# Kernel optimization log

Measured on AMD Instinct MI355X. Metric: run time of the kernel, lower is better.

Reference implementation:

```python
import jax, jax.numpy as jnp
import numpy as np

B, D, H = 16384, 32, 512


def _init_linear(key, fan_in, fan_out):
    k1, k2 = jax.random.split(key)
    lim = 1.0 / np.sqrt(fan_in)
    W = jax.random.uniform(k1, (fan_in, fan_out), jnp.float32, -lim, lim)
    b = jax.random.uniform(k2, (fan_out,), jnp.float32, -lim, lim)
    return W, b


def setup_inputs() -> dict:
    key = jax.random.key(0)
    ks = jax.random.split(key, 8)
    q = jax.random.normal(ks[0], (B, D), jnp.float32)
    p = jax.random.normal(ks[1], (B, D), jnp.float32)
    t = jax.random.uniform(ks[2], (B, 1), jnp.float32)
    dt = jnp.float32(0.1)
    W0, b0 = _init_linear(ks[3], D + 1, H)
    W1, b1 = _init_linear(ks[4], H + 1, H)
    W2, b2 = _init_linear(ks[5], H + 1, H)
    W3, b3 = _init_linear(ks[6], H + 1, H)
    Wout, bout = _init_linear(ks[7], H + 1, D * D)
    return {"q": q, "p": p, "t": t, "dt": dt,
            "W0": W0, "b0": b0, "W1": W1, "b1": b1, "W2": W2, "b2": b2,
            "W3": W3, "b3": b3, "Wout": Wout, "bout": bout}


def _time_injection_net(x, t, Ws, bs):
    # concat time each layer, selu on all but last (matches TimeInjectionNet.forward)
    n = len(Ws)
    for i, (W, b) in enumerate(zip(Ws, bs)):
        x = jnp.concatenate((x, t), axis=1)
        x = x @ W + b
        if i < n - 1:
            x = jax.nn.selu(x)
    return x


def reference(q, p, t, dt, W0, b0, W1, b1, W2, b2, W3, b3, Wout, bout):
    # Q-term integrate_step: matrix from p, integrate q
    Ws = (W0, W1, W2, W3, Wout)
    bs = (b0, b1, b2, b3, bout)
    flat = _time_injection_net(p, t, Ws, bs)           # [B, D*D]
    dense = jnp.clip(flat.reshape(-1, D, D), -20.0, 20.0)  # [B, D, D]
    expm = jax.vmap(jax.scipy.linalg.expm)(dt * dense)  # batched matrix exponential
    new_q = jnp.einsum('bij,bj->bi', expm, q)           # [B, D]
    dlogp = dt * jnp.trace(dense, axis1=1, axis2=2)     # [B]
    return new_q, dlogp
```

## Files before the change

kernel.cpp:

```cpp
#include <hip/hip_runtime.h>
#include <hip/hip_bf16.h>
#include <math.h>

#define BTOT 16384

typedef __attribute__((ext_vector_type(8))) short short8;
typedef __attribute__((ext_vector_type(4))) float f32x4;
typedef __attribute__((ext_vector_type(16))) float f32x16;

__device__ __forceinline__ float selu_fast(float x) {
  const float scale = 1.0507009873554805f;
  const float alpha = 1.6732632423543772f;
  float e = exp2f(x * 1.44269504088896f);
  float neg = alpha * (e - 1.0f);
  return scale * (x > 0.0f ? x : neg);
}

__device__ __forceinline__ unsigned int bf16u(float x) {
  __hip_bfloat16 h = __float2bfloat16(x);
  return (unsigned int)*reinterpret_cast<unsigned short*>(&h);
}

__global__ __launch_bounds__(256) void prep_kernel(
    const float* __restrict__ W0, unsigned int* __restrict__ Wf0,
    const float* __restrict__ W1, unsigned int* __restrict__ Wf1,
    const float* __restrict__ W2, unsigned int* __restrict__ Wf2,
    const float* __restrict__ W3, unsigned int* __restrict__ Wf3,
    const float* __restrict__ Wout, unsigned int* __restrict__ WfO) {
  __shared__ float tile[32][33];
  const int t = blockIdx.x;
  const float* W;
  unsigned int* Wf;
  int N, TS, kbt, nbt;
  if (t < 16)        { W = W0;   Wf = Wf0; N = 512;  TS = 1;  kbt = 0;       nbt = t; }
  else if (t < 272)  { int u = t - 16;  W = W1;   Wf = Wf1; N = 512;  TS = 16; kbt = u & 15; nbt = u >> 4; }
  else if (t < 528)  { int u = t - 272; W = W2;   Wf = Wf2; N = 512;  TS = 16; kbt = u & 15; nbt = u >> 4; }
  else if (t < 784)  { int u = t - 528; W = W3;   Wf = Wf3; N = 512;  TS = 16; kbt = u & 15; nbt = u >> 4; }
  else               { int u = t - 784; W = Wout; Wf = WfO; N = 1024; TS = 16; kbt = u & 15; nbt = u >> 4; }
  const int kb32 = kbt * 32, nb32 = nbt * 32;
  const int tx = threadIdx.x & 31, ty = threadIdx.x >> 5;
  #pragma unroll
  for (int rr = 0; rr < 4; ++rr) {
    int kl = ty + rr * 8;
    tile[kl][tx] = W[(size_t)(kb32 + kl) * N + nb32 + tx];
  }
  __syncthreads();
  const int cbb = threadIdx.x >> 7;
  const int rest = threadIdx.x & 127;
  const int l = rest >> 1;
  const int wjh = rest & 1;
  const int cb = 2 * nbt + cbb;
  unsigned int wv[2];
  #pragma unroll
  for (int m = 0; m < 2; ++m) {
    int wj = wjh * 2 + m;
    int kl = (l >> 4) * 8 + wj * 2;
    int nl = cbb * 16 + (l & 15);
    wv[m] = bf16u(tile[kl][nl]) | (bf16u(tile[kl + 1][nl]) << 16);
  }
  size_t widx = ((size_t)(cb * TS + kbt) * 64 + l) * 4 + wjh * 2;
  *reinterpret_cast<uint2*>(Wf + widx) = make_uint2(wv[0], wv[1]);
}

template<int K, int N, int MODE>
__device__ __forceinline__ void run_layer(
    const short8* __restrict__ Wf,
    const float* __restrict__ Wlast,
    const float* __restrict__ bias,
    char* actBuf,
    __hip_bfloat16* __restrict__ gOut, int rowbase,
    const float* tsl, int w, int lane) {
  constexpr int TS = K / 32;
  constexpr int NKB = K / 8;
  constexpr int PASSES = N / 512;
  const int colloc = lane & 15, kg = lane >> 4;
  int rbyte[2], rmask[2];
  #pragma unroll
  for (int i = 0; i < 2; ++i) {
    int r = i * 16 + colloc;
    rbyte[i] = r * 1024;
    rmask[i] = r & (NKB - 1);
  }
  #pragma unroll 1
  for (int pass = 0; pass < PASSES; ++pass) {
    const int wb = pass * 512 + w * 32;
    const int cb0 = wb >> 4;
    f32x4 acc[2][2] = {};
    short8 acur[2], bcur0, bcur1;
    bcur0 = Wf[(size_t)(cb0 * TS) * 64 + lane];
    bcur1 = Wf[(size_t)((cb0 + 1) * TS) * 64 + lane];
    #pragma unroll
    for (int i = 0; i < 2; ++i)
      acur[i] = *reinterpret_cast<const short8*>(actBuf + rbyte[i] + ((kg ^ rmask[i]) * 16));
    #pragma unroll 2
    for (int t = 0; t < TS; ++t) {
      const int tn = (t + 1 < TS) ? (t + 1) : t;
      short8 bnx0 = Wf[(size_t)(cb0 * TS + tn) * 64 + lane];
      short8 bnx1 = Wf[(size_t)((cb0 + 1) * TS + tn) * 64 + lane];
      short8 anx[2];
      #pragma unroll
      for (int i = 0; i < 2; ++i)
        anx[i] = *reinterpret_cast<const short8*>(actBuf + rbyte[i] + (((tn * 4 + kg) ^ rmask[i]) * 16));
      #pragma unroll
      for (int i = 0; i < 2; ++i) {
        acc[i][0] = __builtin_amdgcn_mfma_f32_16x16x32_bf16(acur[i], bcur0, acc[i][0], 0, 0, 0);
        acc[i][1] = __builtin_amdgcn_mfma_f32_16x16x32_bf16(acur[i], bcur1, acc[i][1], 0, 0, 0);
      }
      #pragma unroll
      for (int i = 0; i < 2; ++i) acur[i] = anx[i];
      bcur0 = bnx0; bcur1 = bnx1;
    }
    if (MODE == 0) __syncthreads();
    float wl[2], bb[2];
    #pragma unroll
    for (int c = 0; c < 2; ++c) {
      int col = wb + c * 16 + colloc;
      wl[c] = Wlast[col];
      bb[c] = bias[col];
    }
    #pragma unroll
    for (int i = 0; i < 2; ++i) {
      #pragma unroll
      for (int e = 0; e < 4; ++e) {
        int row = i * 16 + kg * 4 + e;
        float tv = tsl[row];
        #pragma unroll
        for (int c = 0; c < 2; ++c) {
          float v = acc[i][c][e] + tv * wl[c] + bb[c];
          if (MODE == 0) {
            v = selu_fast(v);
            int col = wb + c * 16 + colloc;
            int off = row * 1024 + (((col >> 3) ^ (row & 63)) * 16) + (col & 7) * 2;
            *reinterpret_cast<unsigned short*>(actBuf + off) =
                (unsigned short)bf16u(v);
          } else {
            v = fminf(fmaxf(v, -20.f), 20.f);
            float o = __shfl_xor(v, 1);
            unsigned int me = bf16u(v), ot = bf16u(o);
            unsigned int pw = (colloc & 1) ? ((me << 16) | ot) : ((ot << 16) | me);
            const bool iwrite = ((colloc & 1) == (e >> 1));
            int col0 = wb + c * 16 + (colloc & ~1);
            if (iwrite) {
              size_t off = (size_t)(rowbase + row) * N + col0;
              *reinterpret_cast<unsigned int*>(
                  reinterpret_cast<char*>(gOut) + off * 2) = pw;
            }
          }
        }
      }
    }
  }
}

__global__ __launch_bounds__(1024) void fused_mlp_kernel(
    const float* __restrict__ p,
    const float* __restrict__ tvec,
    const short8* Wf0, const short8* Wf1, const short8* Wf2,
    const short8* Wf3, const short8* WfO,
    const float* W0l, const float* b0,
    const float* W1l, const float* b1,
    const float* W2l, const float* b2,
    const float* W3l, const float* b3,
    const float* WOl, const float* bO,
    __hip_bfloat16* __restrict__ flatb) {
  __shared__ char buf[32768];
  __shared__ float tsl[32];
  const int tid = threadIdx.x;
  const int w = tid >> 6, lane = tid & 63;
  const int rowbase = blockIdx.x * 32;

  if (tid < 32) tsl[tid] = tvec[rowbase + tid];
  if (tid < 256) {
    const int r = tid >> 3, g = tid & 7;
    float4 v = *reinterpret_cast<const float4*>(p + (size_t)(rowbase + r) * 32 + g * 4);
    unsigned int lo = bf16u(v.x) | (bf16u(v.y) << 16);
    unsigned int hi = bf16u(v.z) | (bf16u(v.w) << 16);
    int off = r * 1024 + (((g >> 1) ^ (r & 3)) * 16) + (g & 1) * 8;
    *reinterpret_cast<uint2*>(buf + off) = make_uint2(lo, hi);
  }
  __syncthreads();

  run_layer<32, 512, 0>(Wf0, W0l, b0, buf, nullptr, rowbase, tsl, w, lane);
  __syncthreads();
  run_layer<512, 512, 0>(Wf1, W1l, b1, buf, nullptr, rowbase, tsl, w, lane);
  __syncthreads();
  run_layer<512, 512, 0>(Wf2, W2l, b2, buf, nullptr, rowbase, tsl, w, lane);
  __syncthreads();
  run_layer<512, 512, 0>(Wf3, W3l, b3, buf, nullptr, rowbase, tsl, w, lane);
  __syncthreads();
  run_layer<512, 1024, 1>(WfO, WOl, bO, buf, flatb, rowbase, tsl, w, lane);
}

#define WAITLDS asm volatile("s_waitcnt lgkmcnt(0)" ::: "memory")

__device__ __forceinline__ unsigned int bf16r(float x) {
  return (__float_as_uint(x) + 0x8000u) >> 16;
}

__device__ __forceinline__ void d2b_lean(const float (&X)[16], int G, short8 (&bfr)[2]) {
  float rcv[8];
  #pragma unroll
  for (int j = 0; j < 8; ++j) {
    const int hp = j >> 2, tt = j & 3;
    float snd = G ? X[8 * hp + tt] : X[8 * hp + 4 + tt];
    rcv[j] = __shfl_xor(snd, 32);
  }
  #pragma unroll
  for (int h = 0; h < 2; ++h) {
    float r8v[8];
    #pragma unroll
    for (int j2 = 0; j2 < 8; ++j2) {
      if (j2 < 4) r8v[j2] = G ? rcv[4 * h + j2] : X[8 * h + j2];
      else        r8v[j2] = G ? X[8 * h + j2] : rcv[4 * h + j2 - 4];
    }
    union { short8 s8; unsigned int u[4]; } bu;
    #pragma unroll
    for (int j = 0; j < 4; ++j)
      bu.u[j] = bf16r(r8v[2 * j]) | (bf16r(r8v[2 * j + 1]) << 16);
    bfr[h] = bu.s8;
  }
}

__device__ __forceinline__ void d2b_split_lean(const float (&X)[16], int G,
                                               short8 (&bh)[2], short8 (&bl)[2]) {
  float rcv[8];
  #pragma unroll
  for (int j = 0; j < 8; ++j) {
    const int hp = j >> 2, tt = j & 3;
    float snd = G ? X[8 * hp + tt] : X[8 * hp + 4 + tt];
    rcv[j] = __shfl_xor(snd, 32);
  }
  #pragma unroll
  for (int h = 0; h < 2; ++h) {
    float r8v[8];
    #pragma unroll
    for (int j2 = 0; j2 < 8; ++j2) {
      if (j2 < 4) r8v[j2] = G ? rcv[4 * h + j2] : X[8 * h + j2];
      else        r8v[j2] = G ? X[8 * h + j2] : rcv[4 * h + j2 - 4];
    }
    union { short8 s8; unsigned int u[4]; } uh, ul;
    #pragma unroll
    for (int j = 0; j < 4; ++j) {
      unsigned int b0 = __float_as_uint(r8v[2 * j]) & 0xFFFF0000u;
      unsigned int b1 = __float_as_uint(r8v[2 * j + 1]) & 0xFFFF0000u;
      float l0 = r8v[2 * j] - __uint_as_float(b0);
      float l1 = r8v[2 * j + 1] - __uint_as_float(b1);
      uh.u[j] = (b0 >> 16) | b1;
      ul.u[j] = bf16r(l0) | (bf16r(l1) << 16);
    }
    bh[h] = uh.s8;
    bl[h] = ul.s8;
  }
}

union u4s8 { uint4 u4; short8 s8; unsigned int u[4]; };

__global__ __launch_bounds__(256) void expm_ilp2_kernel(
    const __hip_bfloat16* __restrict__ flat,
    const float* __restrict__ q,
    const float* __restrict__ dtp,
    float* __restrict__ out_q,
    float* __restrict__ out_dlogp) {
  __shared__ __align__(16) unsigned int SL[4][2][16][33];
  const int tid = threadIdx.x;
  const int w = tid >> 6, lane = tid & 63;
  const int C = lane & 31, G = lane >> 5;
  const int m0 = blockIdx.x * 8 + w * 2;
  const float dt = dtp[0];

  u4s8 t0[2], t1[2];
  float E[2][16];
  float uu[2];
  int nv[2];

  #pragma unroll
  for (int mm = 0; mm < 2; ++mm) {
    const int m = m0 + mm;
    const uint4* fm = reinterpret_cast<const uint4*>(flat + (size_t)m * 1024);
    uint4 v0 = fm[lane];
    uint4 v1 = fm[lane + 64];
    {
      const int r0 = lane >> 2, kpb = (lane & 3) * 4;
      SL[w][mm][kpb + 0][r0] = v0.x; SL[w][mm][kpb + 1][r0] = v0.y;
      SL[w][mm][kpb + 2][r0] = v0.z; SL[w][mm][kpb + 3][r0] = v0.w;
      SL[w][mm][kpb + 0][r0 + 16] = v1.x; SL[w][mm][kpb + 1][r0 + 16] = v1.y;
      SL[w][mm][kpb + 2][r0 + 16] = v1.z; SL[w][mm][kpb + 3][r0 + 16] = v1.w;
    }
    {
      const char* base = reinterpret_cast<const char*>(flat) + (size_t)m * 2048 + C * 64 + G * 16;
      t0[mm].u4 = *reinterpret_cast<const uint4*>(base);
      t1[mm].u4 = *reinterpret_cast<const uint4*>(base + 32);
    }

    float sa = 0.f;
    #pragma unroll
    for (int i = 0; i < 4; ++i) {
      sa += fabsf(__uint_as_float(t0[mm].u[i] << 16)) + fabsf(__uint_as_float(t0[mm].u[i] & 0xFFFF0000u));
      sa += fabsf(__uint_as_float(t1[mm].u[i] << 16)) + fabsf(__uint_as_float(t1[mm].u[i] & 0xFFFF0000u));
    }
    sa += __shfl_xor(sa, 32);
    float nrm = sa;
    #pragma unroll
    for (int off = 1; off < 32; off <<= 1) nrm = fmaxf(nrm, __shfl_xor(nrm, off));

    int s = 0;
    float anrm = dt * nrm;
    if (anrm > 1.0f) {
      s = (int)ceilf(log2f(anrm));
      s = s < 1 ? 1 : (s > 6 ? 6 : s);
    }
    nv[mm] = 1 << s;
    const float u = dt * exp2f(-(float)s);
    uu[mm] = u;

    unsigned int pt0[4], pt1[4];
    #pragma unroll
    for (int d = 0; d < 4; ++d) {
      pt0[d] = (unsigned int)__shfl_xor((int)t0[mm].u[d], 32);
      pt1[d] = (unsigned int)__shfl_xor((int)t1[mm].u[d], 32);
    }
    float tr = 0.f;
    #pragma unroll
    for (int j = 0; j < 4; ++j) {
      #pragma unroll
      for (int e2 = 0; e2 < 4; ++e2) {
        const int i = 4 * j + e2;
        const int rd = e2 + 8 * j + 4 * G;
        const bool own = ((j & 1) == G);
        unsigned int dwO, dwP;
        if ((e2 >> 1) == 0) {
          dwO = G ? ((j < 2) ? t0[mm].u[2] : t1[mm].u[2]) : ((j < 2) ? t0[mm].u[0] : t1[mm].u[0]);
          dwP = G ? ((j < 2) ? pt0[2] : pt1[2]) : ((j < 2) ? pt0[0] : pt1[0]);
        } else {
          dwO = G ? ((j < 2) ? t0[mm].u[3] : t1[mm].u[3]) : ((j < 2) ? t0[mm].u[1] : t1[mm].u[1]);
          dwP = G ? ((j < 2) ? pt0[3] : pt1[3]) : ((j < 2) ? pt0[1] : pt1[1]);
        }
        unsigned int dw = own ? dwO : dwP;
        unsigned int h16 = (e2 & 1) ? (dw >> 16) : (dw & 0xFFFFu);
        float mv = __uint_as_float(h16 << 16);
        float dI = (rd == C) ? 1.0f : 0.0f;
        E[mm][i] = dI + u * mv;
        tr += dI * mv;
      }
    }
    #pragma unroll
    for (int off = 1; off < 64; off <<= 1) tr += __shfl_xor(tr, off);
    if (lane == 0) out_dlogp[m] = dt * tr;
  }

  WAITLDS;

  short8 Mfr[2][2];
  {
    const unsigned int selpat = (C & 1) ? 0x07060302u : 0x05040100u;
    #pragma unroll
    for (int mm = 0; mm < 2; ++mm) {
      #pragma unroll
      for (int h = 0; h < 2; ++h) {
        unsigned int rr[8];
        #pragma unroll
        for (int e = 0; e < 8; ++e) rr[e] = SL[w][mm][C >> 1][16 * h + 8 * G + e];
        union { short8 s8; unsigned int u[4]; } mu;
        #pragma unroll
        for (int j = 0; j < 4; ++j)
          mu.u[j] = __builtin_amdgcn_perm(rr[2 * j + 1], rr[2 * j], selpat);
        Mfr[mm][h] = mu.s8;
      }
    }
  }

  float Qc[2][16];
  float ck[2];
  #pragma unroll
  for (int mm = 0; mm < 2; ++mm) {
    ck[mm] = uu[mm] * uu[mm] * 0.5f;
    f32x16 acc = {};
    acc = __builtin_amdgcn_mfma_f32_32x32x16_bf16(Mfr[mm][0], t0[mm].s8, acc, 0, 0, 0);
    acc = __builtin_amdgcn_mfma_f32_32x32x16_bf16(Mfr[mm][1], t1[mm].s8, acc, 0, 0, 0);
    #pragma unroll
    for (int i = 0; i < 16; ++i) { Qc[mm][i] = acc[i]; E[mm][i] += ck[mm] * acc[i]; }
  }
  #pragma unroll
  for (int k = 3; k <= 6; ++k) {
    #pragma unroll
    for (int mm = 0; mm < 2; ++mm) {
      short8 bfr[2];
      d2b_lean(Qc[mm], G, bfr);
      f32x16 acc = {};
      acc = __builtin_amdgcn_mfma_f32_32x32x16_bf16(Mfr[mm][0], bfr[0], acc, 0, 0, 0);
      acc = __builtin_amdgcn_mfma_f32_32x32x16_bf16(Mfr[mm][1], bfr[1], acc, 0, 0, 0);
      ck[mm] *= uu[mm] * (1.0f / (float)k);
      #pragma unroll
      for (int i = 0; i < 16; ++i) { Qc[mm][i] = acc[i]; E[mm][i] += ck[mm] * acc[i]; }
    }
  }

  short8 beh[2][2], bel[2][2];
  #pragma unroll
  for (int mm = 0; mm < 2; ++mm)
    d2b_split_lean(E[mm], G, beh[mm], bel[mm]);

  float qv[2];
  qv[0] = q[(size_t)m0 * 32 + C];
  qv[1] = q[(size_t)(m0 + 1) * 32 + C];
  const int nvmax = nv[0] > nv[1] ? nv[0] : nv[1];
  #pragma unroll 1
  for (int it = 0; it < nvmax; ++it) {
    #pragma unroll
    for (int mm = 0; mm < 2; ++mm) {
      unsigned int hb = __float_as_uint(qv[mm]) & 0xFFFF0000u;
      float lof = qv[mm] - __uint_as_float(hb);
      unsigned int pw = (hb >> 16) | (bf16r(lof) << 16);
      short8 vh[2], vl[2];
      #pragma unroll
      for (int h = 0; h < 2; ++h) {
        unsigned int g[8];
        #pragma unroll
        for (int e = 0; e < 8; ++e)
          g[e] = (unsigned int)__shfl((int)pw, 16 * h + 8 * G + e);
        union { short8 s8; unsigned int u[4]; } uh, ul;
        #pragma unroll
        for (int j = 0; j < 4; ++j) {
          uh.u[j] = __builtin_amdgcn_perm(g[2 * j + 1], g[2 * j], 0x05040100u);
          ul.u[j] = __builtin_amdgcn_perm(g[2 * j + 1], g[2 * j], 0x07060302u);
        }
        vh[h] = uh.s8;
        vl[h] = ul.s8;
      }
      f32x16 acc = {};
      acc = __builtin_amdgcn_mfma_f32_32x32x16_bf16(vh[0], beh[mm][0], acc, 0, 0, 0);
      acc = __builtin_amdgcn_mfma_f32_32x32x16_bf16(vh[1], beh[mm][1], acc, 0, 0, 0);
      acc = __builtin_amdgcn_mfma_f32_32x32x16_bf16(vl[0], beh[mm][0], acc, 0, 0, 0);
      acc = __builtin_amdgcn_mfma_f32_32x32x16_bf16(vl[1], beh[mm][1], acc, 0, 0, 0);
      acc = __builtin_amdgcn_mfma_f32_32x32x16_bf16(vh[0], bel[mm][0], acc, 0, 0, 0);
      acc = __builtin_amdgcn_mfma_f32_32x32x16_bf16(vh[1], bel[mm][1], acc, 0, 0, 0);
      qv[mm] = (it < nv[mm]) ? acc[0] : qv[mm];
    }
  }
  if (G == 0) {
    out_q[(size_t)m0 * 32 + C] = qv[0];
    out_q[(size_t)(m0 + 1) * 32 + C] = qv[1];
  }
}

extern "C" void kernel_launch(void* const* d_in, const int* in_sizes, int n_in,
                              void* d_out, int out_size, void* d_ws, size_t ws_size,
                              hipStream_t stream) {
  const float* q    = (const float*)d_in[0];
  const float* p    = (const float*)d_in[1];
  const float* t    = (const float*)d_in[2];
  const float* dt   = (const float*)d_in[3];
  const float* W0   = (const float*)d_in[4];
  const float* b0   = (const float*)d_in[5];
  const float* W1   = (const float*)d_in[6];
  const float* b1   = (const float*)d_in[7];
  const float* W2   = (const float*)d_in[8];
  const float* b2   = (const float*)d_in[9];
  const float* W3   = (const float*)d_in[10];
  const float* b3   = (const float*)d_in[11];
  const float* Wout = (const float*)d_in[12];
  const float* bout = (const float*)d_in[13];

  char* ws = (char*)d_ws;
  __hip_bfloat16* flatb = (__hip_bfloat16*)ws;
  unsigned int* Wf0 = (unsigned int*)(ws + (size_t)BTOT * 1024 * 2);
  unsigned int* Wf1 = Wf0 + 32 * 512 / 2;
  unsigned int* Wf2 = Wf1 + 512 * 512 / 2;
  unsigned int* Wf3 = Wf2 + 512 * 512 / 2;
  unsigned int* WfO = Wf3 + 512 * 512 / 2;

  prep_kernel<<<1296, 256, 0, stream>>>(W0, Wf0, W1, Wf1, W2, Wf2, W3, Wf3,
                                        Wout, WfO);

  fused_mlp_kernel<<<512, 1024, 0, stream>>>(
      p, t,
      (const short8*)Wf0, (const short8*)Wf1, (const short8*)Wf2,
      (const short8*)Wf3, (const short8*)WfO,
      W0 + 32 * 512, b0, W1 + 512 * 512, b1, W2 + 512 * 512, b2,
      W3 + 512 * 512, b3, Wout + 512 * 1024, bout, flatb);

  float* out_q     = (float*)d_out;
  float* out_dlogp = out_q + (size_t)BTOT * 32;
  expm_ilp2_kernel<<<BTOT / 8, 256, 0, stream>>>(flatb, q, dt, out_q, out_dlogp);
}
```

Measured before the change: 119.5 us.

## Fuse MLP and batched matrix exponential into one kernel via LDS handoff

```diff
diff --git a/kernel.cpp b/kernel.cpp
--- a/kernel.cpp
+++ b/kernel.cpp
@@ -20,6 +20,12 @@
   __hip_bfloat16 h = __float2bfloat16(x);
   return (unsigned int)*reinterpret_cast<unsigned short*>(&h);
 }
+
+__device__ __forceinline__ unsigned int bf16r(float x) {
+  return (__float_as_uint(x) + 0x8000u) >> 16;
+}
+
+union u4s8 { uint4 u4; short8 s8; unsigned int u[4]; };
 
 __global__ __launch_bounds__(256) void prep_kernel(
     const float* __restrict__ W0, unsigned int* __restrict__ Wf0,
@@ -67,8 +73,7 @@
     const short8* __restrict__ Wf,
     const float* __restrict__ Wlast,
     const float* __restrict__ bias,
-    char* actBuf,
-    __hip_bfloat16* __restrict__ gOut, int rowbase,
+    char* actBuf, char* flatL,
     const float* tsl, int w, int lane) {
   constexpr int TS = K / 32;
   constexpr int NKB = K / 8;
@@ -140,11 +145,8 @@
             unsigned int pw = (colloc & 1) ? ((me << 16) | ot) : ((ot << 16) | me);
             const bool iwrite = ((colloc & 1) == (e >> 1));
             int col0 = wb + c * 16 + (colloc & ~1);
-            if (iwrite) {
-              size_t off = (size_t)(rowbase + row) * N + col0;
-              *reinterpret_cast<unsigned int*>(
-                  reinterpret_cast<char*>(gOut) + off * 2) = pw;
-            }
+            if (iwrite)
+              *reinterpret_cast<unsigned int*>(flatL + (size_t)row * 2048 + col0 * 2) = pw;
           }
         }
       }
@@ -152,7 +154,65 @@
   }
 }
 
-__global__ __launch_bounds__(1024) void fused_mlp_kernel(
+__device__ __forceinline__ void d2b_lean(const float (&X)[16], int G, short8 (&bfr)[2]) {
+  float rcv[8];
+  #pragma unroll
+  for (int j = 0; j < 8; ++j) {
+    const int hp = j >> 2, tt = j & 3;
+    float snd = G ? X[8 * hp + tt] : X[8 * hp + 4 + tt];
+    rcv[j] = __shfl_xor(snd, 32);
+  }
+  #pragma unroll
+  for (int h = 0; h < 2; ++h) {
+    float r8v[8];
+    #pragma unroll
+    for (int j2 = 0; j2 < 8; ++j2) {
+      if (j2 < 4) r8v[j2] = G ? rcv[4 * h + j2] : X[8 * h + j2];
+      else        r8v[j2] = G ? X[8 * h + j2] : rcv[4 * h + j2 - 4];
+    }
+    union { short8 s8; unsigned int u[4]; } bu;
+    #pragma unroll
+    for (int j = 0; j < 4; ++j)
+      bu.u[j] = bf16r(r8v[2 * j]) | (bf16r(r8v[2 * j + 1]) << 16);
+    bfr[h] = bu.s8;
+  }
+}
+
+__device__ __forceinline__ void d2b_split_lean(const float (&X)[16], int G,
+                                               short8 (&bh)[2], short8 (&bl)[2]) {
+  float rcv[8];
+  #pragma unroll
+  for (int j = 0; j < 8; ++j) {
+    const int hp = j >> 2, tt = j & 3;
+    float snd = G ? X[8 * hp + tt] : X[8 * hp + 4 + tt];
+    rcv[j] = __shfl_xor(snd, 32);
+  }
+  #pragma unroll
+  for (int h = 0; h < 2; ++h) {
+    float r8v[8];
+    #pragma unroll
+    for (int j2 = 0; j2 < 8; ++j2) {
+      if (j2 < 4) r8v[j2] = G ? rcv[4 * h + j2] : X[8 * h + j2];
+      else        r8v[j2] = G ? X[8 * h + j2] : rcv[4 * h + j2 - 4];
+    }
+    union { short8 s8; unsigned int u[4]; } uh, ul;
+    #pragma unroll
+    for (int j = 0; j < 4; ++j) {
+      unsigned int b0 = __float_as_uint(r8v[2 * j]) & 0xFFFF0000u;
+      unsigned int b1 = __float_as_uint(r8v[2 * j + 1]) & 0xFFFF0000u;
+      float l0 = r8v[2 * j] - __uint_as_float(b0);
+      float l1 = r8v[2 * j + 1] - __uint_as_float(b1);
+      uh.u[j] = (b0 >> 16) | b1;
+      ul.u[j] = bf16r(l0) | (bf16r(l1) << 16);
+    }
+    bh[h] = uh.s8;
+    bl[h] = ul.s8;
+  }
+}
+
+#define WAITLDS asm volatile("s_waitcnt lgkmcnt(0)" ::: "memory")
+
+__global__ __launch_bounds__(1024) void mega_kernel(
     const float* __restrict__ p,
     const float* __restrict__ tvec,
     const short8* Wf0, const short8* Wf1, const short8* Wf2,
@@ -162,9 +222,15 @@
     const float* W2l, const float* b2,
     const float* W3l, const float* b3,
     const float* WOl, const float* bO,
-    __hip_bfloat16* __restrict__ flatb) {
-  __shared__ char buf[32768];
+    const float* __restrict__ q,
+    const float* __restrict__ dtp,
+    float* __restrict__ out_q,
+    float* __restrict__ out_dlogp) {
+  __shared__ char actflat[98304];
+  __shared__ __align__(16) unsigned int slab[16 * 16 * 33];
   __shared__ float tsl[32];
+  char* act = actflat;
+  char* flatL = actflat + 32768;
   const int tid = threadIdx.x;
   const int w = tid >> 6, lane = tid & 63;
   const int rowbase = blockIdx.x * 32;
@@ -176,118 +242,47 @@
     unsigned int lo = bf16u(v.x) | (bf16u(v.y) << 16);
     unsigned int hi = bf16u(v.z) | (bf16u(v.w) << 16);
     int off = r * 1024 + (((g >> 1) ^ (r & 3)) * 16) + (g & 1) * 8;
-    *reinterpret_cast<uint2*>(buf + off) = make_uint2(lo, hi);
-  }
-  __syncthreads();
-
-  run_layer<32, 512, 0>(Wf0, W0l, b0, buf, nullptr, rowbase, tsl, w, lane);
-  __syncthreads();
-  run_layer<512, 512, 0>(Wf1, W1l, b1, buf, nullptr, rowbase, tsl, w, lane);
-  __syncthreads();
-  run_layer<512, 512, 0>(Wf2, W2l, b2, buf, nullptr, rowbase, tsl, w, lane);
-  __syncthreads();
-  run_layer<512, 512, 0>(Wf3, W3l, b3, buf, nullptr, rowbase, tsl, w, lane);
-  __syncthreads();
-  run_layer<512, 1024, 1>(WfO, WOl, bO, buf, flatb, rowbase, tsl, w, lane);
-}
-
-#define WAITLDS asm volatile("s_waitcnt lgkmcnt(0)" ::: "memory")
-
-__device__ __forceinline__ unsigned int bf16r(float x) {
-  return (__float_as_uint(x) + 0x8000u) >> 16;
-}
-
-__device__ __forceinline__ void d2b_lean(const float (&X)[16], int G, short8 (&bfr)[2]) {
-  float rcv[8];
-  #pragma unroll
-  for (int j = 0; j < 8; ++j) {
-    const int hp = j >> 2, tt = j & 3;
-    float snd = G ? X[8 * hp + tt] : X[8 * hp + 4 + tt];
-    rcv[j] = __shfl_xor(snd, 32);
-  }
-  #pragma unroll
-  for (int h = 0; h < 2; ++h) {
-    float r8v[8];
-    #pragma unroll
-    for (int j2 = 0; j2 < 8; ++j2) {
-      if (j2 < 4) r8v[j2] = G ? rcv[4 * h + j2] : X[8 * h + j2];
-      else        r8v[j2] = G ? X[8 * h + j2] : rcv[4 * h + j2 - 4];
-    }
-    union { short8 s8; unsigned int u[4]; } bu;
-    #pragma unroll
-    for (int j = 0; j < 4; ++j)
-      bu.u[j] = bf16r(r8v[2 * j]) | (bf16r(r8v[2 * j + 1]) << 16);
-    bfr[h] = bu.s8;
-  }
-}
-
-__device__ __forceinline__ void d2b_split_lean(const float (&X)[16], int G,
-                                               short8 (&bh)[2], short8 (&bl)[2]) {
-  float rcv[8];
-  #pragma unroll
-  for (int j = 0; j < 8; ++j) {
-    const int hp = j >> 2, tt = j & 3;
-    float snd = G ? X[8 * hp + tt] : X[8 * hp + 4 + tt];
-    rcv[j] = __shfl_xor(snd, 32);
-  }
-  #pragma unroll
-  for (int h = 0; h < 2; ++h) {
-    float r8v[8];
-    #pragma unroll
-    for (int j2 = 0; j2 < 8; ++j2) {
-      if (j2 < 4) r8v[j2] = G ? rcv[4 * h + j2] : X[8 * h + j2];
-      else        r8v[j2] = G ? X[8 * h + j2] : rcv[4 * h + j2 - 4];
-    }
-    union { short8 s8; unsigned int u[4]; } uh, ul;
-    #pragma unroll
-    for (int j = 0; j < 4; ++j) {
-      unsigned int b0 = __float_as_uint(r8v[2 * j]) & 0xFFFF0000u;
-      unsigned int b1 = __float_as_uint(r8v[2 * j + 1]) & 0xFFFF0000u;
-      float l0 = r8v[2 * j] - __uint_as_float(b0);
-      float l1 = r8v[2 * j + 1] - __uint_as_float(b1);
-      uh.u[j] = (b0 >> 16) | b1;
-      ul.u[j] = bf16r(l0) | (bf16r(l1) << 16);
-    }
-    bh[h] = uh.s8;
-    bl[h] = ul.s8;
-  }
-}
-
-union u4s8 { uint4 u4; short8 s8; unsigned int u[4]; };
-
-__global__ __launch_bounds__(256) void expm_ilp2_kernel(
-    const __hip_bfloat16* __restrict__ flat,
-    const float* __restrict__ q,
-    const float* __restrict__ dtp,
-    float* __restrict__ out_q,
-    float* __restrict__ out_dlogp) {
-  __shared__ __align__(16) unsigned int SL[4][2][16][33];
-  const int tid = threadIdx.x;
-  const int w = tid >> 6, lane = tid & 63;
+    *reinterpret_cast<uint2*>(act + off) = make_uint2(lo, hi);
+  }
+  __syncthreads();
+
+  run_layer<32, 512, 0>(Wf0, W0l, b0, act, nullptr, tsl, w, lane);
+  __syncthreads();
+  run_layer<512, 512, 0>(Wf1, W1l, b1, act, nullptr, tsl, w, lane);
+  __syncthreads();
+  run_layer<512, 512, 0>(Wf2, W2l, b2, act, nullptr, tsl, w, lane);
+  __syncthreads();
+  run_layer<512, 512, 0>(Wf3, W3l, b3, act, nullptr, tsl, w, lane);
+  __syncthreads();
+  run_layer<512, 1024, 1>(WfO, WOl, bO, act, flatL, tsl, w, lane);
+  __syncthreads();
+
   const int C = lane & 31, G = lane >> 5;
-  const int m0 = blockIdx.x * 8 + w * 2;
   const float dt = dtp[0];
+  unsigned int* SW = slab + w * (16 * 33);
 
   u4s8 t0[2], t1[2];
   float E[2][16];
   float uu[2];
   int nv[2];
+  short8 Mfr[2][2];
 
   #pragma unroll
   for (int mm = 0; mm < 2; ++mm) {
-    const int m = m0 + mm;
-    const uint4* fm = reinterpret_cast<const uint4*>(flat + (size_t)m * 1024);
-    uint4 v0 = fm[lane];
-    uint4 v1 = fm[lane + 64];
+    const int mloc = w * 2 + mm;
+    const int m = rowbase + mloc;
+    const uint4* fmL = reinterpret_cast<const uint4*>(flatL + (size_t)mloc * 2048);
+    uint4 v0 = fmL[lane];
+    uint4 v1 = fmL[lane + 64];
     {
       const int r0 = lane >> 2, kpb = (lane & 3) * 4;
-      SL[w][mm][kpb + 0][r0] = v0.x; SL[w][mm][kpb + 1][r0] = v0.y;
-      SL[w][mm][kpb + 2][r0] = v0.z; SL[w][mm][kpb + 3][r0] = v0.w;
-      SL[w][mm][kpb + 0][r0 + 16] = v1.x; SL[w][mm][kpb + 1][r0 + 16] = v1.y;
-      SL[w][mm][kpb + 2][r0 + 16] = v1.z; SL[w][mm][kpb + 3][r0 + 16] = v1.w;
+      SW[(kpb + 0) * 33 + r0] = v0.x; SW[(kpb + 1) * 33 + r0] = v0.y;
+      SW[(kpb + 2) * 33 + r0] = v0.z; SW[(kpb + 3) * 33 + r0] = v0.w;
+      SW[(kpb + 0) * 33 + r0 + 16] = v1.x; SW[(kpb + 1) * 33 + r0 + 16] = v1.y;
+      SW[(kpb + 2) * 33 + r0 + 16] = v1.z; SW[(kpb + 3) * 33 + r0 + 16] = v1.w;
     }
     {
-      const char* base = reinterpret_cast<const char*>(flat) + (size_t)m * 2048 + C * 64 + G * 16;
+      const char* base = flatL + (size_t)mloc * 2048 + C * 64 + G * 16;
       t0[mm].u4 = *reinterpret_cast<const uint4*>(base);
       t1[mm].u4 = *reinterpret_cast<const uint4*>(base + 32);
     }
@@ -346,20 +341,15 @@
     #pragma unroll
     for (int off = 1; off < 64; off <<= 1) tr += __shfl_xor(tr, off);
     if (lane == 0) out_dlogp[m] = dt * tr;
-  }
-
-  WAITLDS;
-
-  short8 Mfr[2][2];
-  {
-    const unsigned int selpat = (C & 1) ? 0x07060302u : 0x05040100u;
-    #pragma unroll
-    for (int mm = 0; mm < 2; ++mm) {
+
+    WAITLDS;
+    {
+      const unsigned int selpat = (C & 1) ? 0x07060302u : 0x05040100u;
       #pragma unroll
       for (int h = 0; h < 2; ++h) {
         unsigned int rr[8];
         #pragma unroll
-        for (int e = 0; e < 8; ++e) rr[e] = SL[w][mm][C >> 1][16 * h + 8 * G + e];
+        for (int e = 0; e < 8; ++e) rr[e] = SW[(C >> 1) * 33 + 16 * h + 8 * G + e];
         union { short8 s8; unsigned int u[4]; } mu;
         #pragma unroll
         for (int j = 0; j < 4; ++j)
@@ -367,6 +357,7 @@
         Mfr[mm][h] = mu.s8;
       }
     }
+    WAITLDS;
   }
 
   float Qc[2][16];
@@ -401,8 +392,8 @@
     d2b_split_lean(E[mm], G, beh[mm], bel[mm]);
 
   float qv[2];
-  qv[0] = q[(size_t)m0 * 32 + C];
-  qv[1] = q[(size_t)(m0 + 1) * 32 + C];
+  qv[0] = q[(size_t)(rowbase + w * 2) * 32 + C];
+  qv[1] = q[(size_t)(rowbase + w * 2 + 1) * 32 + C];
   const int nvmax = nv[0] > nv[1] ? nv[0] : nv[1];
   #pragma unroll 1
   for (int it = 0; it < nvmax; ++it) {
@@ -438,8 +429,8 @@
     }
   }
   if (G == 0) {
-    out_q[(size_t)m0 * 32 + C] = qv[0];
-    out_q[(size_t)(m0 + 1) * 32 + C] = qv[1];
+    out_q[(size_t)(rowbase + w * 2) * 32 + C] = qv[0];
+    out_q[(size_t)(rowbase + w * 2 + 1) * 32 + C] = qv[1];
   }
 }
 
@@ -461,9 +452,7 @@
   const float* Wout = (const float*)d_in[12];
   const float* bout = (const float*)d_in[13];
 
-  char* ws = (char*)d_ws;
-  __hip_bfloat16* flatb = (__hip_bfloat16*)ws;
-  unsigned int* Wf0 = (unsigned int*)(ws + (size_t)BTOT * 1024 * 2);
+  unsigned int* Wf0 = (unsigned int*)d_ws;
   unsigned int* Wf1 = Wf0 + 32 * 512 / 2;
   unsigned int* Wf2 = Wf1 + 512 * 512 / 2;
   unsigned int* Wf3 = Wf2 + 512 * 512 / 2;
@@ -472,14 +461,14 @@
   prep_kernel<<<1296, 256, 0, stream>>>(W0, Wf0, W1, Wf1, W2, Wf2, W3, Wf3,
                                         Wout, WfO);
 
-  fused_mlp_kernel<<<512, 1024, 0, stream>>>(
+  float* out_q     = (float*)d_out;
+  float* out_dlogp = out_q + (size_t)BTOT * 32;
+
+  mega_kernel<<<512, 1024, 0, stream>>>(
       p, t,
       (const short8*)Wf0, (const short8*)Wf1, (const short8*)Wf2,
       (const short8*)Wf3, (const short8*)WfO,
       W0 + 32 * 512, b0, W1 + 512 * 512, b1, W2 + 512 * 512, b2,
-      W3 + 512 * 512, b3, Wout + 512 * 1024, bout, flatb);
-
-  float* out_q     = (float*)d_out;
-  float* out_dlogp = out_q + (size_t)BTOT * 32;
-  expm_ilp2_kernel<<<BTOT / 8, 256, 0, stream>>>(flatb, q, dt, out_q, out_dlogp);
-}
+      W3 + 512 * 512, b3, Wout + 512 * 1024, bout,
+      q, dt, out_q, out_dlogp);
+}
```

Result: slower. 158.1 us (+32.3%).

## Halve MLP block to 512 threads with each wave computing two column passes

Applied to the files above, without the earlier changes.

```diff
diff --git a/kernel.cpp b/kernel.cpp
--- a/kernel.cpp
+++ b/kernel.cpp
@@ -62,17 +62,15 @@
   *reinterpret_cast<uint2*>(Wf + widx) = make_uint2(wv[0], wv[1]);
 }
 
-template<int K, int N, int MODE>
-__device__ __forceinline__ void run_layer(
+template<int K>
+__device__ __forceinline__ void run_hidden(
     const short8* __restrict__ Wf,
     const float* __restrict__ Wlast,
     const float* __restrict__ bias,
     char* actBuf,
-    __hip_bfloat16* __restrict__ gOut, int rowbase,
     const float* tsl, int w, int lane) {
   constexpr int TS = K / 32;
   constexpr int NKB = K / 8;
-  constexpr int PASSES = N / 512;
   const int colloc = lane & 15, kg = lane >> 4;
   int rbyte[2], rmask[2];
   #pragma unroll
@@ -81,11 +79,11 @@
     rbyte[i] = r * 1024;
     rmask[i] = r & (NKB - 1);
   }
-  #pragma unroll 1
-  for (int pass = 0; pass < PASSES; ++pass) {
-    const int wb = pass * 512 + w * 32;
+  f32x4 acc[2][2][2] = {};
+  #pragma unroll
+  for (int pass = 0; pass < 2; ++pass) {
+    const int wb = pass * 256 + w * 32;
     const int cb0 = wb >> 4;
-    f32x4 acc[2][2] = {};
     short8 acur[2], bcur0, bcur1;
     bcur0 = Wf[(size_t)(cb0 * TS) * 64 + lane];
     bcur1 = Wf[(size_t)((cb0 + 1) * TS) * 64 + lane];
@@ -103,6 +101,82 @@
         anx[i] = *reinterpret_cast<const short8*>(actBuf + rbyte[i] + (((tn * 4 + kg) ^ rmask[i]) * 16));
       #pragma unroll
       for (int i = 0; i < 2; ++i) {
+        acc[pass][i][0] = __builtin_amdgcn_mfma_f32_16x16x32_bf16(acur[i], bcur0, acc[pass][i][0], 0, 0, 0);
+        acc[pass][i][1] = __builtin_amdgcn_mfma_f32_16x16x32_bf16(acur[i], bcur1, acc[pass][i][1], 0, 0, 0);
+      }
+      #pragma unroll
+      for (int i = 0; i < 2; ++i) acur[i] = anx[i];
+      bcur0 = bnx0; bcur1 = bnx1;
+    }
+  }
+  __syncthreads();
+  #pragma unroll
+  for (int pass = 0; pass < 2; ++pass) {
+    const int wb = pass * 256 + w * 32;
+    float wl[2], bb[2];
+    #pragma unroll
+    for (int c = 0; c < 2; ++c) {
+      int col = wb + c * 16 + colloc;
+      wl[c] = Wlast[col];
+      bb[c] = bias[col];
+    }
+    #pragma unroll
+    for (int i = 0; i < 2; ++i) {
+      #pragma unroll
+      for (int e = 0; e < 4; ++e) {
+        int row = i * 16 + kg * 4 + e;
+        float tv = tsl[row];
+        #pragma unroll
+        for (int c = 0; c < 2; ++c) {
+          float v = acc[pass][i][c][e] + tv * wl[c] + bb[c];
+          v = selu_fast(v);
+          int col = wb + c * 16 + colloc;
+          int off = row * 1024 + (((col >> 3) ^ (row & 63)) * 16) + (col & 7) * 2;
+          *reinterpret_cast<unsigned short*>(actBuf + off) = (unsigned short)bf16u(v);
+        }
+      }
+    }
+  }
+}
+
+__device__ __forceinline__ void run_out(
+    const short8* __restrict__ Wf,
+    const float* __restrict__ Wlast,
+    const float* __restrict__ bias,
+    const char* actBuf,
+    __hip_bfloat16* __restrict__ gOut, int rowbase,
+    const float* tsl, int w, int lane) {
+  constexpr int K = 512, TS = K / 32, NKB = K / 8;
+  const int colloc = lane & 15, kg = lane >> 4;
+  int rbyte[2], rmask[2];
+  #pragma unroll
+  for (int i = 0; i < 2; ++i) {
+    int r = i * 16 + colloc;
+    rbyte[i] = r * 1024;
+    rmask[i] = r & (NKB - 1);
+  }
+  #pragma unroll 1
+  for (int pass = 0; pass < 4; ++pass) {
+    const int wb = pass * 256 + w * 32;
+    const int cb0 = wb >> 4;
+    f32x4 acc[2][2] = {};
+    short8 acur[2], bcur0, bcur1;
+    bcur0 = Wf[(size_t)(cb0 * TS) * 64 + lane];
+    bcur1 = Wf[(size_t)((cb0 + 1) * TS) * 64 + lane];
+    #pragma unroll
+    for (int i = 0; i < 2; ++i)
+      acur[i] = *reinterpret_cast<const short8*>(actBuf + rbyte[i] + ((kg ^ rmask[i]) * 16));
+    #pragma unroll 2
+    for (int t = 0; t < TS; ++t) {
+      const int tn = (t + 1 < TS) ? (t + 1) : t;
+      short8 bnx0 = Wf[(size_t)(cb0 * TS + tn) * 64 + lane];
+      short8 bnx1 = Wf[(size_t)((cb0 + 1) * TS + tn) * 64 + lane];
+      short8 anx[2];
+      #pragma unroll
+      for (int i = 0; i < 2; ++i)
+        anx[i] = *reinterpret_cast<const short8*>(actBuf + rbyte[i] + (((tn * 4 + kg) ^ rmask[i]) * 16));
+      #pragma unroll
+      for (int i = 0; i < 2; ++i) {
         acc[i][0] = __builtin_amdgcn_mfma_f32_16x16x32_bf16(acur[i], bcur0, acc[i][0], 0, 0, 0);
         acc[i][1] = __builtin_amdgcn_mfma_f32_16x16x32_bf16(acur[i], bcur1, acc[i][1], 0, 0, 0);
       }
@@ -110,7 +184,6 @@
       for (int i = 0; i < 2; ++i) acur[i] = anx[i];
       bcur0 = bnx0; bcur1 = bnx1;
     }
-    if (MODE == 0) __syncthreads();
     float wl[2], bb[2];
     #pragma unroll
     for (int c = 0; c < 2; ++c) {
@@ -127,24 +200,16 @@
         #pragma unroll
         for (int c = 0; c < 2; ++c) {
           float v = acc[i][c][e] + tv * wl[c] + bb[c];
-          if (MODE == 0) {
-            v = selu_fast(v);
-            int col = wb + c * 16 + colloc;
-            int off = row * 1024 + (((col >> 3) ^ (row & 63)) * 16) + (col & 7) * 2;
-            *reinterpret_cast<unsigned short*>(actBuf + off) =
-                (unsigned short)bf16u(v);
-          } else {
-            v = fminf(fmaxf(v, -20.f), 20.f);
-            float o = __shfl_xor(v, 1);
-            unsigned int me = bf16u(v), ot = bf16u(o);
-            unsigned int pw = (colloc & 1) ? ((me << 16) | ot) : ((ot << 16) | me);
-            const bool iwrite = ((colloc & 1) == (e >> 1));
-            int col0 = wb + c * 16 + (colloc & ~1);
-            if (iwrite) {
-              size_t off = (size_t)(rowbase + row) * N + col0;
-              *reinterpret_cast<unsigned int*>(
-                  reinterpret_cast<char*>(gOut) + off * 2) = pw;
-            }
+          v = fminf(fmaxf(v, -20.f), 20.f);
+          float o = __shfl_xor(v, 1);
+          unsigned int me = bf16u(v), ot = bf16u(o);
+          unsigned int pw = (colloc & 1) ? ((me << 16) | ot) : ((ot << 16) | me);
+          const bool iwrite = ((colloc & 1) == (e >> 1));
+          int col0 = wb + c * 16 + (colloc & ~1);
+          if (iwrite) {
+            size_t off = (size_t)(rowbase + row) * 1024 + col0;
+            *reinterpret_cast<unsigned int*>(
+                reinterpret_cast<char*>(gOut) + off * 2) = pw;
           }
         }
       }
@@ -152,7 +217,7 @@
   }
 }
 
-__global__ __launch_bounds__(1024) void fused_mlp_kernel(
+__global__ __launch_bounds__(512) void fused_mlp_kernel(
     const float* __restrict__ p,
     const float* __restrict__ tvec,
     const short8* Wf0, const short8* Wf1, const short8* Wf2,
@@ -180,15 +245,15 @@
   }
   __syncthreads();
 
-  run_layer<32, 512, 0>(Wf0, W0l, b0, buf, nullptr, rowbase, tsl, w, lane);
-  __syncthreads();
-  run_layer<512, 512, 0>(Wf1, W1l, b1, buf, nullptr, rowbase, tsl, w, lane);
-  __syncthreads();
-  run_layer<512, 512, 0>(Wf2, W2l, b2, buf, nullptr, rowbase, tsl, w, lane);
-  __syncthreads();
-  run_layer<512, 512, 0>(Wf3, W3l, b3, buf, nullptr, rowbase, tsl, w, lane);
-  __syncthreads();
-  run_layer<512, 1024, 1>(WfO, WOl, bO, buf, flatb, rowbase, tsl, w, lane);
+  run_hidden<32>(Wf0, W0l, b0, buf, tsl, w, lane);
+  __syncthreads();
+  run_hidden<512>(Wf1, W1l, b1, buf, tsl, w, lane);
+  __syncthreads();
+  run_hidden<512>(Wf2, W2l, b2, buf, tsl, w, lane);
+  __syncthreads();
+  run_hidden<512>(Wf3, W3l, b3, buf, tsl, w, lane);
+  __syncthreads();
+  run_out(WfO, WOl, bO, buf, flatb, rowbase, tsl, w, lane);
 }
 
 #define WAITLDS asm volatile("s_waitcnt lgkmcnt(0)" ::: "memory")
@@ -472,7 +537,7 @@
   prep_kernel<<<1296, 256, 0, stream>>>(W0, Wf0, W1, Wf1, W2, Wf2, W3, Wf3,
                                         Wout, WfO);
 
-  fused_mlp_kernel<<<512, 1024, 0, stream>>>(
+  fused_mlp_kernel<<<512, 512, 0, stream>>>(
       p, t,
       (const short8*)Wf0, (const short8*)Wf1, (const short8*)Wf2,
       (const short8*)Wf3, (const short8*)WfO,
```

Result: faster. 106.1 us, median of 2 (-11.2%).
